# Optimization experiments

Hardware: AMD Instinct MI355X
Metric: run time of the kernel (lower is better)

## Reference

```python
import jax, jax.numpy as jnp
import numpy as np

EPS = 1e-4  # performer softmax-kernel epsilon


def _orthogonal_projection(nb_rows, nb_cols, seed=0):
    # gaussian_orthogonal_random_matrix with scaling=0: stacked QR blocks
    # scaled by chi-distributed row norms of a fresh gaussian matrix.
    rng = np.random.default_rng(seed)
    n_blocks = int(np.ceil(nb_rows / nb_cols))
    blocks = []
    for _ in range(n_blocks):
        g = rng.standard_normal((nb_cols, nb_cols))
        qmat, _ = np.linalg.qr(g)
        blocks.append(qmat.T)  # rows are orthonormal
    qstack = np.concatenate(blocks, axis=0)[:nb_rows]
    multiplier = np.linalg.norm(rng.standard_normal((nb_rows, nb_cols)), axis=1)
    return (multiplier[:, None] * qstack).astype(np.float32)


def setup_inputs() -> dict:
    key = jax.random.key(0)
    kq, kk, kv = jax.random.split(key, 3)
    B, H, N, D = 2, 8, 16384, 64
    M = 266  # int(D * log(D))
    return {
        "q": jax.random.normal(kq, (B, H, N, D), dtype=jnp.float32),
        "k": jax.random.normal(kk, (B, H, N, D), dtype=jnp.float32),
        "v": jax.random.normal(kv, (B, H, N, D), dtype=jnp.float32),
        "projection": jnp.asarray(_orthogonal_projection(M, D)),
    }


def softmax_kernel(x, projection, is_query):
    # FAVOR+ positive softmax random features.
    d = x.shape[-1]
    m = projection.shape[0]
    data_normalizer = d ** -0.25
    ratio = m ** -0.5
    # [B,H,N,M]
    data_dash = jnp.einsum('bhnd,md->bhnm', x * data_normalizer, projection)
    diag_data = 0.5 * (data_normalizer ** 2) * jnp.sum(x * x, axis=-1, keepdims=True)
    if is_query:
        stab = jnp.max(data_dash, axis=-1, keepdims=True)
    else:
        stab = jnp.max(data_dash, axis=(-2, -1), keepdims=True)
    stab = jax.lax.stop_gradient(stab)  # torch detaches the max
    return ratio * (jnp.exp(data_dash - diag_data - stab) + EPS)


def linear_attention(qp, kp, v):
    # qp,kp: [B,H,N,M]; v: [B,H,N,D]
    k_cumsum = jnp.sum(kp, axis=-2)                                # [B,H,M]
    d_inv = 1.0 / jnp.einsum('bhnm,bhm->bhn', qp, k_cumsum)        # [B,H,N]
    context = jnp.einsum('bhnm,bhnd->bhmd', kp, v)                 # [B,H,M,D]
    return jnp.einsum('bhnm,bhmd,bhn->bhnd', qp, context, d_inv)   # [B,H,N,D]


def reference(q, k, v, projection):
    qp = softmax_kernel(q, projection, is_query=True)
    kp = softmax_kernel(k, projection, is_query=False)
    return linear_attention(qp, kp, v)
```

## Files before the change

### kernel.cpp

```cpp
#include <hip/hip_runtime.h>
#include <hip/hip_bf16.h>
#include <math.h>

#define BHN 16
#define NN 16384
#define DD 64
#define MM 266
#define MP 272
#define CTS 288

constexpr float DN    = 0.35355339059327373f;
constexpr float HDN2  = 0.0625f;
constexpr float RATIO = 0.0613139339f;
constexpr float EPSF  = 1e-4f;

#define WS_STAB 0
#define WS_PART 16
#define WS_KC   1040
#define WS_KCS  5648
#define WS_CTXS 24080
#define CTX_SLICE (BHN * MP * DD)
#define KC_SLICE  (BHN * CTS)
#define WS_VD   1138192
#define WS_CD   1139216
#define WS_KSUM 1140240
#define WS_PBH  1140256
#define WS_CTH  1157664
#define ZERO_OFF 5648
#define ZERO_CNT 1133568

typedef __attribute__((ext_vector_type(8))) short s16x8;
typedef __attribute__((ext_vector_type(4))) float f32x4;

#define MFMA(acc, a, b) acc = __builtin_amdgcn_mfma_f32_16x16x32_bf16(a, b, acc, 0, 0, 0)

__device__ __forceinline__ float bf2f_u(unsigned short h) {
  union { unsigned u; float f; } v; v.u = ((unsigned)h) << 16; return v.f;
}
__device__ __forceinline__ unsigned pk_bf16(float a, float b) {
  float2 f; f.x = a; f.y = b;
  __hip_bfloat162 h = __float22bfloat162_rn(f);
  union { __hip_bfloat162 h; unsigned u; } c; c.h = h;
  return c.u;
}
__device__ __forceinline__ void split8(const float* v, s16x8& hi, s16x8& lo) {
  union U { s16x8 s; unsigned u[4]; } H, L;
#pragma unroll
  for (int i = 0; i < 4; i++) {
    float a = v[2 * i], b = v[2 * i + 1];
    unsigned uh = pk_bf16(a, b);
    H.u[i] = uh;
    float r0 = a - bf2f_u((unsigned short)(uh & 0xffffu));
    float r1 = b - bf2f_u((unsigned short)(uh >> 16));
    L.u[i] = pk_bf16(r0, r1);
  }
  hi = H.s; lo = L.s;
}
__device__ __forceinline__ void split8g(const float* __restrict__ p,
                                        s16x8& hi, s16x8& lo, float& ss) {
  float4 f0 = *(const float4*)p;
  float4 f1 = *(const float4*)(p + 4);
  float v[8] = {f0.x, f0.y, f0.z, f0.w, f1.x, f1.y, f1.z, f1.w};
#pragma unroll
  for (int i = 0; i < 8; i++) ss += v[i] * v[i];
  split8(v, hi, lo);
}
__device__ __forceinline__ void split8l(const float* p, s16x8& hi, s16x8& lo) {
  float4 f0 = *(const float4*)p;
  float4 f1 = *(const float4*)(p + 4);
  float v[8] = {f0.x, f0.y, f0.z, f0.w, f1.x, f1.y, f1.z, f1.w};
  split8(v, hi, lo);
}

__global__ void prep_kernel(const float* __restrict__ P,
                            unsigned short* __restrict__ pbh,
                            unsigned short* __restrict__ pbl) {
  int idx = blockIdx.x * 256 + threadIdx.x;
  if (idx < MP * DD) {
    float f = (idx < MM * DD) ? P[idx] : 0.f;
    unsigned short h = (unsigned short)(pk_bf16(f, 0.f) & 0xffffu);
    pbh[idx] = h;
    pbl[idx] = (unsigned short)(pk_bf16(f - bf2f_u(h), 0.f) & 0xffffu);
  }
}

__global__ __launch_bounds__(256) void ctx_kernel(
    const float* __restrict__ K, const float* __restrict__ V,
    const unsigned short* __restrict__ pbh, const unsigned short* __restrict__ pbl,
    float* __restrict__ ws) {
  __shared__ float vT[64 * 36];
  __shared__ float kpb[MP * 36];
  __shared__ float redm[4];
  const int tid = threadIdx.x;
  const int wave = tid >> 6, lane = tid & 63;
  const int l15 = lane & 15, quad = lane >> 4;
  const int bh = blockIdx.x;
  const int slice = blockIdx.y & 3;
  float* ctxs = ws + WS_CTXS + (size_t)slice * CTX_SLICE;
  float* kcs  = ws + WS_KCS + slice * KC_SLICE;
  f32x4 zero4 = {0.f, 0.f, 0.f, 0.f};
  f32x4 acc[5][4];
#pragma unroll
  for (int i = 0; i < 5; i++)
#pragma unroll
    for (int j = 0; j < 4; j++) acc[i][j] = zero4;
  float kcp[5] = {0.f, 0.f, 0.f, 0.f, 0.f};
  float vsum[8] = {0.f, 0.f, 0.f, 0.f, 0.f, 0.f, 0.f, 0.f};
  float mxk = -1e30f;

  for (int it = 0; it < 16; it++) {
    const int n0 = blockIdx.y * 512 + it * 32;
#pragma unroll
    for (int j = 0; j < 2; j++) {
      const int n = tid & 31;
      const int d4 = ((tid >> 5) + j * 8) * 4;
      float4 vv = *(const float4*)(V + ((size_t)(bh * NN + n0 + n)) * DD + d4);
      vT[(d4 + 0) * 36 + n] = vv.x;
      vT[(d4 + 1) * 36 + n] = vv.y;
      vT[(d4 + 2) * 36 + n] = vv.z;
      vT[(d4 + 3) * 36 + n] = vv.w;
      vsum[j * 4 + 0] += vv.x;
      vsum[j * 4 + 1] += vv.y;
      vsum[j * 4 + 2] += vv.z;
      vsum[j * 4 + 3] += vv.w;
    }
    s16x8 ah[2][2], al[2][2];
    float dg[2][4];
#pragma unroll
    for (int g = 0; g < 2; g++) {
      float ss = 0.f;
#pragma unroll
      for (int s = 0; s < 2; s++)
        split8g(K + ((size_t)(bh * NN + n0 + g * 16 + l15)) * DD + s * 32 + quad * 8,
                ah[g][s], al[g][s], ss);
      ss += __shfl_xor(ss, 16);
      ss += __shfl_xor(ss, 32);
#pragma unroll
      for (int r = 0; r < 4; r++) dg[g][r] = HDN2 * __shfl(ss, quad * 4 + r);
    }
#pragma unroll 5
    for (int ti = 0; ti < 5; ti++) {
      const int t = wave + ti * 4;
      if (t < 17) {
        f32x4 dd[2] = {zero4, zero4};
#pragma unroll
        for (int s = 0; s < 2; s++) {
          s16x8 b8h = *(const s16x8*)(pbh + (t * 16 + l15) * DD + s * 32 + quad * 8);
          s16x8 b8l = *(const s16x8*)(pbl + (t * 16 + l15) * DD + s * 32 + quad * 8);
#pragma unroll
          for (int g = 0; g < 2; g++) {
            MFMA(dd[g], ah[g][s], b8h); MFMA(dd[g], al[g][s], b8h); MFMA(dd[g], ah[g][s], b8l);
          }
        }
        const bool pad = (t == 16 && l15 >= 10);
#pragma unroll
        for (int g = 0; g < 2; g++) {
          float4 kp;
          float* kpp = (float*)&kp;
#pragma unroll
          for (int r = 0; r < 4; r++) {
            kpp[r] = __expf(DN * dd[g][r] - dg[g][r]);
            if (!pad) mxk = fmaxf(mxk, dd[g][r]);
          }
          if (pad) { kp.x = kp.y = kp.z = kp.w = 0.f; }
          kcp[ti] += kpp[0] + kpp[1] + kpp[2] + kpp[3];
          *(float4*)(kpb + (t * 16 + l15) * 36 + g * 16 + quad * 4) = kp;
        }
      }
    }
    __syncthreads();
    s16x8 vbh[4], vbl[4];
#pragma unroll
    for (int dt = 0; dt < 4; dt++)
      split8l(vT + (dt * 16 + l15) * 36 + quad * 8, vbh[dt], vbl[dt]);
#pragma unroll 5
    for (int ti = 0; ti < 5; ti++) {
      const int t = wave + ti * 4;
      if (t < 17) {
        s16x8 kah, kal;
        split8l(kpb + (t * 16 + l15) * 36 + quad * 8, kah, kal);
#pragma unroll
        for (int dt = 0; dt < 4; dt++) {
          MFMA(acc[ti][dt], kah, vbh[dt]);
          MFMA(acc[ti][dt], kal, vbh[dt]);
          MFMA(acc[ti][dt], kah, vbl[dt]);
        }
      }
    }
    __syncthreads();
  }
#pragma unroll 5
  for (int ti = 0; ti < 5; ti++) {
    const int t = wave + ti * 4;
    if (t < 17) {
      float kc = kcp[ti];
      kc += __shfl_xor(kc, 16);
      kc += __shfl_xor(kc, 32);
      if (lane < 16) atomicAdd(&kcs[bh * CTS + t * 16 + lane], kc);
#pragma unroll
      for (int dt = 0; dt < 4; dt++)
#pragma unroll
        for (int r = 0; r < 4; r++) {
          int m = t * 16 + quad * 4 + r;
          atomicAdd(&ctxs[((size_t)(bh * MP + m)) * DD + dt * 16 + l15], acc[ti][dt][r]);
        }
    }
  }
#pragma unroll
  for (int j = 0; j < 2; j++)
#pragma unroll
    for (int c = 0; c < 4; c++) {
      float s = vsum[j * 4 + c];
      s += __shfl_xor(s, 1);  s += __shfl_xor(s, 2);  s += __shfl_xor(s, 4);
      s += __shfl_xor(s, 8);  s += __shfl_xor(s, 16);
      if ((tid & 31) == 0)
        atomicAdd(&ws[WS_VD + bh * 64 + ((tid >> 5) + j * 8) * 4 + c], s);
    }
#pragma unroll
  for (int d = 1; d < 64; d <<= 1) mxk = fmaxf(mxk, __shfl_xor(mxk, d));
  if (lane == 0) redm[wave] = mxk;
  __syncthreads();
  if (tid == 0)
    ws[WS_PART + bh * 64 + blockIdx.y] =
        fmaxf(fmaxf(redm[0], redm[1]), fmaxf(redm[2], redm[3]));
}

__global__ void stab_kernel(float* __restrict__ ws) {
  const int bh = blockIdx.x, lane = threadIdx.x;
  float m = (lane < 32) ? ws[WS_PART + bh * 64 + lane] : -1e30f;
#pragma unroll
  for (int d = 1; d < 64; d <<= 1) m = fmaxf(m, __shfl_xor(m, d));
  if (lane == 0) ws[WS_STAB + bh] = DN * m;
}

__global__ __launch_bounds__(256) void ctxt_kernel(
    float* __restrict__ ws, unsigned short* __restrict__ cth,
    unsigned short* __restrict__ ctl) {
  const int bh = blockIdx.x;
  const int idx = blockIdx.y * 256 + threadIdx.x;
  const int d = idx / CTS, m = idx % CTS;
  const float stab = ws[WS_STAB + bh];
  const float scale = RATIO * __expf(-stab);
  const float reps  = RATIO * EPSF;
  float f = 0.f;
  if (m < MP) {
#pragma unroll
    for (int s = 0; s < 4; s++)
      f += ws[WS_CTXS + (size_t)s * CTX_SLICE + ((size_t)(bh * MP + m)) * DD + d];
  }
  float ctxf = (m < MM) ? (scale * f + reps * ws[WS_VD + bh * 64 + d]) : 0.f;
  unsigned short h = (unsigned short)(pk_bf16(ctxf, 0.f) & 0xffffu);
  cth[((size_t)(bh * DD) + d) * CTS + m] = h;
  ctl[((size_t)(bh * DD) + d) * CTS + m] =
      (unsigned short)(pk_bf16(ctxf - bf2f_u(h), 0.f) & 0xffffu);
  if (d == 0) {
    float kc = 0.f;
    if (m < MM) {
      float kr = 0.f;
#pragma unroll
      for (int s = 0; s < 4; s++) kr += ws[WS_KCS + s * KC_SLICE + bh * CTS + m];
      kc = scale * kr + reps * (float)NN;
    }
    ws[WS_KC + bh * CTS + m] = kc;
  }
}

__global__ __launch_bounds__(256) void csum_kernel(
    const unsigned short* __restrict__ cth, const unsigned short* __restrict__ ctl,
    float* __restrict__ ws) {
  const int bh = blockIdx.x, t = threadIdx.x;
  const int d = t >> 2, p = t & 3;
  const unsigned short* rh = cth + ((size_t)(bh * DD) + d) * CTS;
  const unsigned short* rl = ctl + ((size_t)(bh * DD) + d) * CTS;
  float s = 0.f;
  for (int i = 0; i < 68; i++) {
    int m = p * 68 + i;
    s += bf2f_u(rh[m]) + bf2f_u(rl[m]);
  }
  s += __shfl_xor(s, 1);
  s += __shfl_xor(s, 2);
  if (p == 0) ws[WS_CD + bh * 64 + d] = s;
  if (t < 64) {
    float kk = 0.f;
    for (int m = t; m < MM; m += 64) kk += ws[WS_KC + bh * CTS + m];
#pragma unroll
    for (int dd2 = 1; dd2 < 64; dd2 <<= 1) kk += __shfl_xor(kk, dd2);
    if (t == 0) ws[WS_KSUM + bh] = kk;
  }
}

__global__ __launch_bounds__(256) void out_kernel(
    const float* __restrict__ Q, const unsigned short* __restrict__ pbh,
    const unsigned short* __restrict__ pbl, const unsigned short* __restrict__ cth,
    const unsigned short* __restrict__ ctl, const float* __restrict__ ws,
    float* __restrict__ Out) {
  __shared__ float qpb[4][2][16 * 36];
  const int tid = threadIdx.x;
  const int wave = tid >> 6, lane = tid & 63;
  const int l15 = lane & 15, quad = lane >> 4;
  const int bh = blockIdx.x;
  const int n0 = blockIdx.y * 128 + wave * 32;
  f32x4 zero4 = {0.f, 0.f, 0.f, 0.f};
  s16x8 ah[2][2], al[2][2];
  float sub[2][4];
#pragma unroll
  for (int g = 0; g < 2; g++) {
    float ss = 0.f;
#pragma unroll
    for (int s = 0; s < 2; s++)
      split8g(Q + ((size_t)(bh * NN + n0 + g * 16 + l15)) * DD + s * 32 + quad * 8,
              ah[g][s], al[g][s], ss);
    ss += __shfl_xor(ss, 16);
    ss += __shfl_xor(ss, 32);
#pragma unroll
    for (int r = 0; r < 4; r++) sub[g][r] = HDN2 * __shfl(ss, quad * 4 + r);
  }
  f32x4 oa[2][4];
#pragma unroll
  for (int g = 0; g < 2; g++)
#pragma unroll
    for (int dt = 0; dt < 4; dt++) oa[g][dt] = zero4;
  float dn[2][4] = {{0.f,0.f,0.f,0.f},{0.f,0.f,0.f,0.f}};
  float mx[2][4] = {{-1e30f,-1e30f,-1e30f,-1e30f},{-1e30f,-1e30f,-1e30f,-1e30f}};
  for (int s9 = 0; s9 < 9; s9++) {
#pragma unroll
    for (int u = 0; u < 2; u++) {
      const int t = s9 * 2 + u;
      if (t < 17) {
        f32x4 dd[2] = {zero4, zero4};
#pragma unroll
        for (int s = 0; s < 2; s++) {
          s16x8 b8h = *(const s16x8*)(pbh + (t * 16 + l15) * DD + s * 32 + quad * 8);
          s16x8 b8l = *(const s16x8*)(pbl + (t * 16 + l15) * DD + s * 32 + quad * 8);
#pragma unroll
          for (int g = 0; g < 2; g++) {
            MFMA(dd[g], ah[g][s], b8h); MFMA(dd[g], al[g][s], b8h); MFMA(dd[g], ah[g][s], b8l);
          }
        }
        const float kcv = ws[WS_KC + bh * CTS + t * 16 + l15];
        const bool pad = (t == 16 && l15 >= 10);
#pragma unroll
        for (int g = 0; g < 2; g++)
#pragma unroll
          for (int r = 0; r < 4; r++) {
            float dv = dd[g][r];
            if (!pad) mx[g][r] = fmaxf(mx[g][r], dv);
            float w = __expf(DN * dv - sub[g][r]);
            if (pad) w = 0.f;
            dn[g][r] += w * kcv;
            qpb[wave][g][(quad * 4 + r) * 36 + u * 16 + l15] = w;
          }
      } else {
#pragma unroll
        for (int g = 0; g < 2; g++)
#pragma unroll
          for (int r = 0; r < 4; r++) qpb[wave][g][(quad * 4 + r) * 36 + 16 + l15] = 0.f;
      }
    }
    s16x8 qah[2], qal[2];
#pragma unroll
    for (int g = 0; g < 2; g++)
      split8l(qpb[wave][g] + l15 * 36 + quad * 8, qah[g], qal[g]);
#pragma unroll
    for (int dt = 0; dt < 4; dt++) {
      s16x8 c8h = *(const s16x8*)(cth + ((size_t)(bh * DD + dt * 16 + l15)) * CTS + s9 * 32 + quad * 8);
      s16x8 c8l = *(const s16x8*)(ctl + ((size_t)(bh * DD + dt * 16 + l15)) * CTS + s9 * 32 + quad * 8);
#pragma unroll
      for (int g = 0; g < 2; g++) {
        MFMA(oa[g][dt], qah[g], c8h);
        MFMA(oa[g][dt], qal[g], c8h);
        MFMA(oa[g][dt], qah[g], c8l);
      }
    }
  }
  const float kcsum = ws[WS_KSUM + bh];
  float er[2][4];
#pragma unroll
  for (int g = 0; g < 2; g++)
#pragma unroll
    for (int r = 0; r < 4; r++) {
#pragma unroll
      for (int d = 1; d < 16; d <<= 1) {
        dn[g][r] += __shfl_xor(dn[g][r], d);
        mx[g][r] = fmaxf(mx[g][r], __shfl_xor(mx[g][r], d));
      }
      float e = EPSF * __expf(DN * mx[g][r]);
      er[g][r] = e;
      dn[g][r] = 1.0f / (dn[g][r] + e * kcsum);
    }
#pragma unroll
  for (int g = 0; g < 2; g++)
#pragma unroll
    for (int dt = 0; dt < 4; dt++) {
      const float cdv = ws[WS_CD + bh * 64 + dt * 16 + l15];
#pragma unroll
      for (int r = 0; r < 4; r++)
        Out[((size_t)(bh * NN + n0 + g * 16 + quad * 4 + r)) * DD + dt * 16 + l15] =
            (oa[g][dt][r] + er[g][r] * cdv) * dn[g][r];
    }
}

extern "C" void kernel_launch(void* const* d_in, const int* in_sizes, int n_in,
                              void* d_out, int out_size, void* d_ws, size_t ws_size,
                              hipStream_t stream) {
  const float* q = (const float*)d_in[0];
  const float* k = (const float*)d_in[1];
  const float* v = (const float*)d_in[2];
  const float* p = (const float*)d_in[3];
  float* out = (float*)d_out;
  float* ws  = (float*)d_ws;
  unsigned short* pbh = (unsigned short*)(ws + WS_PBH);
  unsigned short* pbl = pbh + MP * DD;
  unsigned short* cth = (unsigned short*)(ws + WS_CTH);
  unsigned short* ctl = cth + (size_t)BHN * DD * CTS;

  hipMemsetAsync(ws + ZERO_OFF, 0, (size_t)ZERO_CNT * sizeof(float), stream);
  prep_kernel<<<68, 256, 0, stream>>>(p, pbh, pbl);
  ctx_kernel<<<dim3(BHN, 32), 256, 0, stream>>>(k, v, pbh, pbl, ws);
  stab_kernel<<<BHN, 64, 0, stream>>>(ws);
  ctxt_kernel<<<dim3(BHN, 72), 256, 0, stream>>>(ws, cth, ctl);
  csum_kernel<<<BHN, 256, 0, stream>>>(cth, ctl, ws);
  out_kernel<<<dim3(BHN, 128), 256, 0, stream>>>(q, pbh, pbl, cth, ctl, ws, out);
}
```

Baseline: 439.9 us.

## Feed K-features from registers directly into context MFMA, drop LDS staging

The exponentiated K random features are now packed to bf16 hi/lo in registers and fed straight into the context MFMA. A matching permuted V operand layout replaces the shared-memory kpb buffer and one barrier per iteration. The grid doubles to 64 blocks per head with half the sequence each, and V is double-buffered. The separate stab kernel is folded into ctxt_kernel via a wave-level max reduction. This cuts LDS traffic and a launch, at the cost of more atomic context accumulations.

```diff
diff --git a/kernel.cpp b/kernel.cpp
--- a/kernel.cpp
+++ b/kernel.cpp
@@ -88,8 +88,7 @@
     const float* __restrict__ K, const float* __restrict__ V,
     const unsigned short* __restrict__ pbh, const unsigned short* __restrict__ pbl,
     float* __restrict__ ws) {
-  __shared__ float vT[64 * 36];
-  __shared__ float kpb[MP * 36];
+  __shared__ float vT[2][64 * 36];
   __shared__ float redm[4];
   const int tid = threadIdx.x;
   const int wave = tid >> 6, lane = tid & 63;
@@ -108,17 +107,18 @@
   float vsum[8] = {0.f, 0.f, 0.f, 0.f, 0.f, 0.f, 0.f, 0.f};
   float mxk = -1e30f;
 
-  for (int it = 0; it < 16; it++) {
-    const int n0 = blockIdx.y * 512 + it * 32;
+  for (int it = 0; it < 8; it++) {
+    const int n0 = blockIdx.y * 256 + it * 32;
+    float* vTp = vT[it & 1];
 #pragma unroll
     for (int j = 0; j < 2; j++) {
       const int n = tid & 31;
       const int d4 = ((tid >> 5) + j * 8) * 4;
       float4 vv = *(const float4*)(V + ((size_t)(bh * NN + n0 + n)) * DD + d4);
-      vT[(d4 + 0) * 36 + n] = vv.x;
-      vT[(d4 + 1) * 36 + n] = vv.y;
-      vT[(d4 + 2) * 36 + n] = vv.z;
-      vT[(d4 + 3) * 36 + n] = vv.w;
+      vTp[(d4 + 0) * 36 + n] = vv.x;
+      vTp[(d4 + 1) * 36 + n] = vv.y;
+      vTp[(d4 + 2) * 36 + n] = vv.z;
+      vTp[(d4 + 3) * 36 + n] = vv.w;
       vsum[j * 4 + 0] += vv.x;
       vsum[j * 4 + 1] += vv.y;
       vsum[j * 4 + 2] += vv.z;
@@ -138,6 +138,16 @@
 #pragma unroll
       for (int r = 0; r < 4; r++) dg[g][r] = HDN2 * __shfl(ss, quad * 4 + r);
     }
+    __syncthreads();
+    s16x8 vbh[4], vbl[4];
+#pragma unroll
+    for (int dt = 0; dt < 4; dt++) {
+      const float* row = vTp + (dt * 16 + l15) * 36 + quad * 4;
+      float4 f0 = *(const float4*)row;
+      float4 f1 = *(const float4*)(row + 16);
+      float v8[8] = {f0.x, f0.y, f0.z, f0.w, f1.x, f1.y, f1.z, f1.w};
+      split8(v8, vbh[dt], vbl[dt]);
+    }
 #pragma unroll 5
     for (int ti = 0; ti < 5; ti++) {
       const int t = wave + ti * 4;
@@ -153,41 +163,42 @@
           }
         }
         const bool pad = (t == 16 && l15 >= 10);
-#pragma unroll
-        for (int g = 0; g < 2; g++) {
-          float4 kp;
-          float* kpp = (float*)&kp;
+        float kp[2][4];
+#pragma unroll
+        for (int g = 0; g < 2; g++)
 #pragma unroll
           for (int r = 0; r < 4; r++) {
-            kpp[r] = __expf(DN * dd[g][r] - dg[g][r]);
+            kp[g][r] = __expf(DN * dd[g][r] - dg[g][r]);
             if (!pad) mxk = fmaxf(mxk, dd[g][r]);
           }
-          if (pad) { kp.x = kp.y = kp.z = kp.w = 0.f; }
-          kcp[ti] += kpp[0] + kpp[1] + kpp[2] + kpp[3];
-          *(float4*)(kpb + (t * 16 + l15) * 36 + g * 16 + quad * 4) = kp;
+        if (pad) {
+#pragma unroll
+          for (int g = 0; g < 2; g++)
+#pragma unroll
+            for (int r = 0; r < 4; r++) kp[g][r] = 0.f;
+        }
+        kcp[ti] += kp[0][0] + kp[0][1] + kp[0][2] + kp[0][3] +
+                   kp[1][0] + kp[1][1] + kp[1][2] + kp[1][3];
+        union { s16x8 s; unsigned u[4]; } KH, KL;
+#pragma unroll
+        for (int g = 0; g < 2; g++)
+#pragma unroll
+          for (int h2 = 0; h2 < 2; h2++) {
+            float a = kp[g][2 * h2], b = kp[g][2 * h2 + 1];
+            unsigned uh = pk_bf16(a, b);
+            KH.u[g * 2 + h2] = uh;
+            float r0 = a - bf2f_u((unsigned short)(uh & 0xffffu));
+            float r1 = b - bf2f_u((unsigned short)(uh >> 16));
+            KL.u[g * 2 + h2] = pk_bf16(r0, r1);
+          }
+#pragma unroll
+        for (int dt = 0; dt < 4; dt++) {
+          MFMA(acc[ti][dt], KH.s, vbh[dt]);
+          MFMA(acc[ti][dt], KL.s, vbh[dt]);
+          MFMA(acc[ti][dt], KH.s, vbl[dt]);
         }
       }
     }
-    __syncthreads();
-    s16x8 vbh[4], vbl[4];
-#pragma unroll
-    for (int dt = 0; dt < 4; dt++)
-      split8l(vT + (dt * 16 + l15) * 36 + quad * 8, vbh[dt], vbl[dt]);
-#pragma unroll 5
-    for (int ti = 0; ti < 5; ti++) {
-      const int t = wave + ti * 4;
-      if (t < 17) {
-        s16x8 kah, kal;
-        split8l(kpb + (t * 16 + l15) * 36 + quad * 8, kah, kal);
-#pragma unroll
-        for (int dt = 0; dt < 4; dt++) {
-          MFMA(acc[ti][dt], kah, vbh[dt]);
-          MFMA(acc[ti][dt], kal, vbh[dt]);
-          MFMA(acc[ti][dt], kah, vbl[dt]);
-        }
-      }
-    }
-    __syncthreads();
   }
 #pragma unroll 5
   for (int ti = 0; ti < 5; ti++) {
@@ -225,21 +236,16 @@
         fmaxf(fmaxf(redm[0], redm[1]), fmaxf(redm[2], redm[3]));
 }
 
-__global__ void stab_kernel(float* __restrict__ ws) {
-  const int bh = blockIdx.x, lane = threadIdx.x;
-  float m = (lane < 32) ? ws[WS_PART + bh * 64 + lane] : -1e30f;
-#pragma unroll
-  for (int d = 1; d < 64; d <<= 1) m = fmaxf(m, __shfl_xor(m, d));
-  if (lane == 0) ws[WS_STAB + bh] = DN * m;
-}
-
 __global__ __launch_bounds__(256) void ctxt_kernel(
     float* __restrict__ ws, unsigned short* __restrict__ cth,
     unsigned short* __restrict__ ctl) {
   const int bh = blockIdx.x;
   const int idx = blockIdx.y * 256 + threadIdx.x;
   const int d = idx / CTS, m = idx % CTS;
-  const float stab = ws[WS_STAB + bh];
+  float pm = ws[WS_PART + bh * 64 + (threadIdx.x & 63)];
+#pragma unroll
+  for (int dd2 = 1; dd2 < 64; dd2 <<= 1) pm = fmaxf(pm, __shfl_xor(pm, dd2));
+  const float stab = DN * pm;
   const float scale = RATIO * __expf(-stab);
   const float reps  = RATIO * EPSF;
   float f = 0.f;
@@ -416,8 +422,7 @@
 
   hipMemsetAsync(ws + ZERO_OFF, 0, (size_t)ZERO_CNT * sizeof(float), stream);
   prep_kernel<<<68, 256, 0, stream>>>(p, pbh, pbl);
-  ctx_kernel<<<dim3(BHN, 32), 256, 0, stream>>>(k, v, pbh, pbl, ws);
-  stab_kernel<<<BHN, 64, 0, stream>>>(ws);
+  ctx_kernel<<<dim3(BHN, 64), 256, 0, stream>>>(k, v, pbh, pbl, ws);
   ctxt_kernel<<<dim3(BHN, 72), 256, 0, stream>>>(ws, cth, ctl);
   csum_kernel<<<BHN, 256, 0, stream>>>(cth, ctl, ws);
   out_kernel<<<dim3(BHN, 128), 256, 0, stream>>>(q, pbh, pbl, cth, ctl, ws, out);
```

After: 514.4 us. +16.9%, slower.

## Widen ctx kernel to 8 waves and fold stab/csum kernels into ctxt

Applied to the files above, without the earlier changes.

The ctx kernel now runs 512 threads (8 waves), so each wave handles at most 3 of the 17 M-tiles instead of 5, and each thread transposes one V float4 per iteration instead of two. The separate stab and csum kernels are removed. The stabilizer max is recomputed inside ctxt, and ctxt accumulates the context column sums and the k-sum through atomics, with the zeroed workspace range extended to cover them. This cuts two launches and the re-read of the bf16 context, at the cost of more atomics and a different summation order for the column sums.

```diff
diff --git a/kernel.cpp b/kernel.cpp
--- a/kernel.cpp
+++ b/kernel.cpp
@@ -27,7 +27,7 @@
 #define WS_PBH  1140256
 #define WS_CTH  1157664
 #define ZERO_OFF 5648
-#define ZERO_CNT 1133568
+#define ZERO_CNT 1134608
 
 typedef __attribute__((ext_vector_type(8))) short s16x8;
 typedef __attribute__((ext_vector_type(4))) float f32x4;
@@ -84,13 +84,13 @@
   }
 }
 
-__global__ __launch_bounds__(256) void ctx_kernel(
+__global__ __launch_bounds__(512, 4) void ctx_kernel(
     const float* __restrict__ K, const float* __restrict__ V,
     const unsigned short* __restrict__ pbh, const unsigned short* __restrict__ pbl,
     float* __restrict__ ws) {
   __shared__ float vT[64 * 36];
   __shared__ float kpb[MP * 36];
-  __shared__ float redm[4];
+  __shared__ float redm[8];
   const int tid = threadIdx.x;
   const int wave = tid >> 6, lane = tid & 63;
   const int l15 = lane & 15, quad = lane >> 4;
@@ -98,31 +98,27 @@
   const int slice = blockIdx.y & 3;
   float* ctxs = ws + WS_CTXS + (size_t)slice * CTX_SLICE;
   float* kcs  = ws + WS_KCS + slice * KC_SLICE;
+  const int vn = tid & 31;
+  const int vd4 = (tid >> 5) * 4;
   f32x4 zero4 = {0.f, 0.f, 0.f, 0.f};
-  f32x4 acc[5][4];
-#pragma unroll
-  for (int i = 0; i < 5; i++)
+  f32x4 acc[3][4];
+#pragma unroll
+  for (int i = 0; i < 3; i++)
 #pragma unroll
     for (int j = 0; j < 4; j++) acc[i][j] = zero4;
-  float kcp[5] = {0.f, 0.f, 0.f, 0.f, 0.f};
-  float vsum[8] = {0.f, 0.f, 0.f, 0.f, 0.f, 0.f, 0.f, 0.f};
+  float kcp[3] = {0.f, 0.f, 0.f};
+  float vsum[4] = {0.f, 0.f, 0.f, 0.f};
   float mxk = -1e30f;
 
   for (int it = 0; it < 16; it++) {
     const int n0 = blockIdx.y * 512 + it * 32;
-#pragma unroll
-    for (int j = 0; j < 2; j++) {
-      const int n = tid & 31;
-      const int d4 = ((tid >> 5) + j * 8) * 4;
-      float4 vv = *(const float4*)(V + ((size_t)(bh * NN + n0 + n)) * DD + d4);
-      vT[(d4 + 0) * 36 + n] = vv.x;
-      vT[(d4 + 1) * 36 + n] = vv.y;
-      vT[(d4 + 2) * 36 + n] = vv.z;
-      vT[(d4 + 3) * 36 + n] = vv.w;
-      vsum[j * 4 + 0] += vv.x;
-      vsum[j * 4 + 1] += vv.y;
-      vsum[j * 4 + 2] += vv.z;
-      vsum[j * 4 + 3] += vv.w;
+    {
+      float4 vv = *(const float4*)(V + ((size_t)(bh * NN + n0 + vn)) * DD + vd4);
+      vT[(vd4 + 0) * 36 + vn] = vv.x;
+      vT[(vd4 + 1) * 36 + vn] = vv.y;
+      vT[(vd4 + 2) * 36 + vn] = vv.z;
+      vT[(vd4 + 3) * 36 + vn] = vv.w;
+      vsum[0] += vv.x; vsum[1] += vv.y; vsum[2] += vv.z; vsum[3] += vv.w;
     }
     s16x8 ah[2][2], al[2][2];
     float dg[2][4];
@@ -138,9 +134,9 @@
 #pragma unroll
       for (int r = 0; r < 4; r++) dg[g][r] = HDN2 * __shfl(ss, quad * 4 + r);
     }
-#pragma unroll 5
-    for (int ti = 0; ti < 5; ti++) {
-      const int t = wave + ti * 4;
+#pragma unroll 3
+    for (int ti = 0; ti < 3; ti++) {
+      const int t = wave + ti * 8;
       if (t < 17) {
         f32x4 dd[2] = {zero4, zero4};
 #pragma unroll
@@ -173,9 +169,9 @@
 #pragma unroll
     for (int dt = 0; dt < 4; dt++)
       split8l(vT + (dt * 16 + l15) * 36 + quad * 8, vbh[dt], vbl[dt]);
-#pragma unroll 5
-    for (int ti = 0; ti < 5; ti++) {
-      const int t = wave + ti * 4;
+#pragma unroll 3
+    for (int ti = 0; ti < 3; ti++) {
+      const int t = wave + ti * 8;
       if (t < 17) {
         s16x8 kah, kal;
         split8l(kpb + (t * 16 + l15) * 36 + quad * 8, kah, kal);
@@ -189,9 +185,9 @@
     }
     __syncthreads();
   }
-#pragma unroll 5
-  for (int ti = 0; ti < 5; ti++) {
-    const int t = wave + ti * 4;
+#pragma unroll 3
+  for (int ti = 0; ti < 3; ti++) {
+    const int t = wave + ti * 8;
     if (t < 17) {
       float kc = kcp[ti];
       kc += __shfl_xor(kc, 16);
@@ -207,39 +203,38 @@
     }
   }
 #pragma unroll
-  for (int j = 0; j < 2; j++)
-#pragma unroll
-    for (int c = 0; c < 4; c++) {
-      float s = vsum[j * 4 + c];
-      s += __shfl_xor(s, 1);  s += __shfl_xor(s, 2);  s += __shfl_xor(s, 4);
-      s += __shfl_xor(s, 8);  s += __shfl_xor(s, 16);
-      if ((tid & 31) == 0)
-        atomicAdd(&ws[WS_VD + bh * 64 + ((tid >> 5) + j * 8) * 4 + c], s);
-    }
+  for (int c = 0; c < 4; c++) {
+    float s = vsum[c];
+    s += __shfl_xor(s, 1);  s += __shfl_xor(s, 2);  s += __shfl_xor(s, 4);
+    s += __shfl_xor(s, 8);  s += __shfl_xor(s, 16);
+    if ((tid & 31) == 0)
+      atomicAdd(&ws[WS_VD + bh * 64 + vd4 + c], s);
+  }
 #pragma unroll
   for (int d = 1; d < 64; d <<= 1) mxk = fmaxf(mxk, __shfl_xor(mxk, d));
   if (lane == 0) redm[wave] = mxk;
   __syncthreads();
-  if (tid == 0)
-    ws[WS_PART + bh * 64 + blockIdx.y] =
-        fmaxf(fmaxf(redm[0], redm[1]), fmaxf(redm[2], redm[3]));
-}
-
-__global__ void stab_kernel(float* __restrict__ ws) {
-  const int bh = blockIdx.x, lane = threadIdx.x;
-  float m = (lane < 32) ? ws[WS_PART + bh * 64 + lane] : -1e30f;
-#pragma unroll
-  for (int d = 1; d < 64; d <<= 1) m = fmaxf(m, __shfl_xor(m, d));
-  if (lane == 0) ws[WS_STAB + bh] = DN * m;
+  if (tid == 0) {
+    float m = redm[0];
+#pragma unroll
+    for (int w = 1; w < 8; w++) m = fmaxf(m, redm[w]);
+    ws[WS_PART + bh * 64 + blockIdx.y] = m;
+  }
 }
 
 __global__ __launch_bounds__(256) void ctxt_kernel(
     float* __restrict__ ws, unsigned short* __restrict__ cth,
     unsigned short* __restrict__ ctl) {
+  __shared__ float cdl[4][64];
   const int bh = blockIdx.x;
-  const int idx = blockIdx.y * 256 + threadIdx.x;
-  const int d = idx / CTS, m = idx % CTS;
-  const float stab = ws[WS_STAB + bh];
+  const int tid = threadIdx.x;
+  const int d = tid & 63;
+  const int mo = tid >> 6;
+  const int m = blockIdx.y * 4 + mo;
+  float pm = (d < 32) ? ws[WS_PART + bh * 64 + d] : -1e30f;
+#pragma unroll
+  for (int dd2 = 1; dd2 < 64; dd2 <<= 1) pm = fmaxf(pm, __shfl_xor(pm, dd2));
+  const float stab = DN * pm;
   const float scale = RATIO * __expf(-stab);
   const float reps  = RATIO * EPSF;
   float f = 0.f;
@@ -253,43 +248,27 @@
   cth[((size_t)(bh * DD) + d) * CTS + m] = h;
   ctl[((size_t)(bh * DD) + d) * CTS + m] =
       (unsigned short)(pk_bf16(ctxf - bf2f_u(h), 0.f) & 0xffffu);
-  if (d == 0) {
+  cdl[mo][d] = ctxf;
+  __syncthreads();
+  if (tid < 64) {
+    float s = cdl[0][tid] + cdl[1][tid] + cdl[2][tid] + cdl[3][tid];
+    atomicAdd(&ws[WS_CD + bh * 64 + tid], s);
+  }
+  if (tid < 4) {
+    const int mk = blockIdx.y * 4 + tid;
     float kc = 0.f;
-    if (m < MM) {
+    if (mk < MM) {
       float kr = 0.f;
 #pragma unroll
-      for (int s = 0; s < 4; s++) kr += ws[WS_KCS + s * KC_SLICE + bh * CTS + m];
+      for (int s = 0; s < 4; s++) kr += ws[WS_KCS + s * KC_SLICE + bh * CTS + mk];
       kc = scale * kr + reps * (float)NN;
-    }
-    ws[WS_KC + bh * CTS + m] = kc;
-  }
-}
-
-__global__ __launch_bounds__(256) void csum_kernel(
-    const unsigned short* __restrict__ cth, const unsigned short* __restrict__ ctl,
-    float* __restrict__ ws) {
-  const int bh = blockIdx.x, t = threadIdx.x;
-  const int d = t >> 2, p = t & 3;
-  const unsigned short* rh = cth + ((size_t)(bh * DD) + d) * CTS;
-  const unsigned short* rl = ctl + ((size_t)(bh * DD) + d) * CTS;
-  float s = 0.f;
-  for (int i = 0; i < 68; i++) {
-    int m = p * 68 + i;
-    s += bf2f_u(rh[m]) + bf2f_u(rl[m]);
-  }
-  s += __shfl_xor(s, 1);
-  s += __shfl_xor(s, 2);
-  if (p == 0) ws[WS_CD + bh * 64 + d] = s;
-  if (t < 64) {
-    float kk = 0.f;
-    for (int m = t; m < MM; m += 64) kk += ws[WS_KC + bh * CTS + m];
-#pragma unroll
-    for (int dd2 = 1; dd2 < 64; dd2 <<= 1) kk += __shfl_xor(kk, dd2);
-    if (t == 0) ws[WS_KSUM + bh] = kk;
-  }
-}
-
-__global__ __launch_bounds__(256) void out_kernel(
+      atomicAdd(&ws[WS_KSUM + bh], kc);
+    }
+    ws[WS_KC + bh * CTS + mk] = kc;
+  }
+}
+
+__global__ __launch_bounds__(256, 4) void out_kernel(
     const float* __restrict__ Q, const unsigned short* __restrict__ pbh,
     const unsigned short* __restrict__ pbl, const unsigned short* __restrict__ cth,
     const unsigned short* __restrict__ ctl, const float* __restrict__ ws,
@@ -416,9 +395,7 @@
 
   hipMemsetAsync(ws + ZERO_OFF, 0, (size_t)ZERO_CNT * sizeof(float), stream);
   prep_kernel<<<68, 256, 0, stream>>>(p, pbh, pbl);
-  ctx_kernel<<<dim3(BHN, 32), 256, 0, stream>>>(k, v, pbh, pbl, ws);
-  stab_kernel<<<BHN, 64, 0, stream>>>(ws);
+  ctx_kernel<<<dim3(BHN, 32), 512, 0, stream>>>(k, v, pbh, pbl, ws);
   ctxt_kernel<<<dim3(BHN, 72), 256, 0, stream>>>(ws, cth, ctl);
-  csum_kernel<<<BHN, 256, 0, stream>>>(cth, ctl, ws);
   out_kernel<<<dim3(BHN, 128), 256, 0, stream>>>(q, pbh, pbl, cth, ctl, ws, out);
 }
```

After: 686.5 us. 1.56x slower.
